# Kernel optimization log

Hardware: AMD Instinct MI355X
Metric: run time of the kernel (lower is better)

The kernel has to match this reference:

```python
import jax, jax.numpy as jnp
import numpy as np

B, T, C = 16, 4096, 128
CODEBOOK_SIZE = 1024


def setup_inputs() -> dict:
    key = jax.random.key(0)
    kx, ke = jax.random.split(key)
    x = jax.random.normal(kx, (B, T, C), dtype=jnp.float32)
    embed = jax.random.normal(ke, (CODEBOOK_SIZE, C), dtype=jnp.float32)
    return {"x": x, "embed": embed}


def reference(x, embed):
    # x: [B, T, C], embed: [K, C]
    b, t, c = x.shape
    flat = x.reshape(b * t, c)                      # [BT, C]
    # distance = -||x - e||^2, expanded so we never materialize [BT, K, C]
    x_sq = jnp.sum(flat * flat, axis=-1, keepdims=True)   # [BT, 1]
    e_sq = jnp.sum(embed * embed, axis=-1)                 # [K]
    dist = 2.0 * (flat @ embed.T) - x_sq - e_sq[None, :]   # [BT, K]
    embed_ind = jnp.argmax(dist, axis=-1).reshape(b, t)    # [B, T]
    quantized = embed[embed_ind]                           # [B, T, C] gather
    return quantized, embed_ind
```

## Files before the change

kernel.cpp:

```cpp
#include <hip/hip_runtime.h>
#include <float.h>


#define Cdim        128
#define KCODES      1024
#define CH          32
#define NCH         32
#define BROWS       128
#define THREADS     256
#define IMG_OFF     4096
#define CHUNK_BYTES 16384

typedef _Float16 f16;
typedef __attribute__((ext_vector_type(8))) _Float16 f16x8;
typedef __attribute__((ext_vector_type(4))) float    f32x4;

#define MFMA16(A, B, C) __builtin_amdgcn_mfma_f32_16x16x32_f16((A), (B), (C), 0, 0, 0)

__global__ __launch_bounds__(256) void esq_kernel(const float* __restrict__ embed,
                                                  float* __restrict__ esq, int K) {
    int gid  = blockIdx.x * blockDim.x + threadIdx.x;
    int code = gid >> 6;
    int lane = threadIdx.x & 63;
    if (code >= K) return;
    float2 v = ((const float2*)(embed + (size_t)code * Cdim))[lane];
    float  s = fmaf(v.x, v.x, v.y * v.y);
    #pragma unroll
    for (int m = 32; m >= 1; m >>= 1) s += __shfl_xor(s, m, 64);
    if (lane == 0) esq[code] = s;
}

__device__ __forceinline__ void cvt8s(float4 a, float4 b, float scale,
                                      f16x8& h, f16x8& lo) {
    float v[8] = {a.x, a.y, a.z, a.w, b.x, b.y, b.z, b.w};
    #pragma unroll
    for (int i = 0; i < 8; ++i) {
        float s = v[i] * scale;
        f16 hh = (f16)s;
        h[i]  = hh;
        lo[i] = (f16)(s - (float)hh);
    }
}

__global__ __launch_bounds__(256) void bconv_kernel(const float* __restrict__ embed,
                                                    char* __restrict__ ws) {
    int t    = blockIdx.x * 256 + threadIdx.x;
    int code = t >> 4;
    int seg  = t & 15;
    int ks   = seg >> 2;
    int kseg = seg & 3;
    int ch = code >> 5, ct = (code >> 4) & 1, lr = code & 15;
    const float4* p = (const float4*)(embed + (size_t)code * Cdim + ks * 32 + kseg * 8);
    f16x8 h, lo;
    cvt8s(p[0], p[1], 1.0f, h, lo);
    size_t base = (size_t)IMG_OFF + (size_t)ch * CHUNK_BYTES
                + (ct * 4 + ks) * 1024 + (kseg * 16 + lr) * 16;
    *(f16x8*)(ws + base)        = h;
    *(f16x8*)(ws + base + 8192) = lo;
}

__device__ __forceinline__ void gll16(const void* g, void* l) {
    __builtin_amdgcn_global_load_lds(
        (const __attribute__((address_space(1))) unsigned int*)g,
        (__attribute__((address_space(3))) unsigned int*)l, 16, 0, 0);
}

__global__ __launch_bounds__(THREADS, 2) void vq_kernel(
    const float* __restrict__ x, const float* __restrict__ embed,
    const char* __restrict__ ws, float* __restrict__ outq,
    float* __restrict__ outi) {

    __shared__ __align__(16) char Bb[3][CHUNK_BYTES];

    const int tid  = threadIdx.x;
    const int wid  = tid >> 6;
    const int l    = tid & 63;
    const int lr   = l & 15;
    const int lg   = l >> 4;
    const int row0 = blockIdx.x * BROWS;
    const int wrow = row0 + wid * 32;

    #pragma unroll
    for (int b = 0; b < 2; ++b) {
        const char* src = ws + IMG_OFF + b * CHUNK_BYTES + wid * 4096 + (size_t)l * 16;
        char*       dst = &Bb[b][wid * 4096];
        #pragma unroll
        for (int i = 0; i < 4; ++i) gll16(src + i * 1024, dst + i * 1024);
    }

    f16x8 bxh[2][4], bxl[2][4];
    #pragma unroll
    for (int rt = 0; rt < 2; ++rt) {
        const float* xr = x + (size_t)(wrow + rt * 16 + lr) * Cdim + lg * 8;
        #pragma unroll
        for (int ks = 0; ks < 4; ++ks) {
            float4 v0 = *(const float4*)(xr + ks * 32);
            float4 v1 = *(const float4*)(xr + ks * 32 + 4);
            cvt8s(v0, v1, 2.0f, bxh[rt][ks], bxl[rt][ks]);
        }
    }

    const float* esqp = (const float*)ws;

    float best[2] = {-FLT_MAX, -FLT_MAX};
    int   bidx[2] = {0, 0};
    int cur = 0, pf = 2;

    #pragma unroll 1
    for (int ch = 0; ch < NCH; ++ch) {
        if (ch == NCH - 1) asm volatile("s_waitcnt vmcnt(0)" ::: "memory");
        else               asm volatile("s_waitcnt vmcnt(4)" ::: "memory");
        __builtin_amdgcn_s_barrier();

        if (ch + 2 < NCH) {
            const char* src = ws + IMG_OFF + (size_t)(ch + 2) * CHUNK_BYTES
                            + wid * 4096 + (size_t)l * 16;
            char* dst = &Bb[0][0] + (size_t)pf * CHUNK_BYTES + wid * 4096;
            #pragma unroll
            for (int i = 0; i < 4; ++i) gll16(src + i * 1024, dst + i * 1024);
        }

        f32x4 acc[2][2];
        #pragma unroll
        for (int ct = 0; ct < 2; ++ct)
            #pragma unroll
            for (int rt = 0; rt < 2; ++rt)
                acc[ct][rt] = (f32x4){0.f, 0.f, 0.f, 0.f};

        const char* bb = &Bb[0][0] + (size_t)cur * CHUNK_BYTES + (size_t)l * 16;

        #pragma unroll
        for (int ks = 0; ks < 4; ++ks) {
            f16x8 eh0 = *(const f16x8*)(bb + ks * 1024);
            f16x8 el0 = *(const f16x8*)(bb + ks * 1024 + 8192);
            f16x8 eh1 = *(const f16x8*)(bb + (4 + ks) * 1024);
            f16x8 el1 = *(const f16x8*)(bb + (4 + ks) * 1024 + 8192);

            __builtin_amdgcn_s_setprio(1);
            acc[0][0] = MFMA16(eh0, bxh[0][ks], acc[0][0]);
            acc[0][1] = MFMA16(eh0, bxh[1][ks], acc[0][1]);
            acc[1][0] = MFMA16(eh1, bxh[0][ks], acc[1][0]);
            acc[1][1] = MFMA16(eh1, bxh[1][ks], acc[1][1]);
            acc[0][0] = MFMA16(eh0, bxl[0][ks], acc[0][0]);
            acc[0][1] = MFMA16(eh0, bxl[1][ks], acc[0][1]);
            acc[1][0] = MFMA16(eh1, bxl[0][ks], acc[1][0]);
            acc[1][1] = MFMA16(eh1, bxl[1][ks], acc[1][1]);
            acc[0][0] = MFMA16(el0, bxh[0][ks], acc[0][0]);
            acc[0][1] = MFMA16(el0, bxh[1][ks], acc[0][1]);
            acc[1][0] = MFMA16(el1, bxh[0][ks], acc[1][0]);
            acc[1][1] = MFMA16(el1, bxh[1][ks], acc[1][1]);
            __builtin_amdgcn_s_setprio(0);
        }

        #pragma unroll
        for (int ct = 0; ct < 2; ++ct) {
            const int cb = ch * CH + ct * 16 + lg * 4;
            float4 e4 = *(const float4*)(esqp + cb);
            #pragma unroll
            for (int rt = 0; rt < 2; ++rt)
                #pragma unroll
                for (int j = 0; j < 4; ++j) {
                    float s = acc[ct][rt][j] - ((const float*)&e4)[j];
                    if (s > best[rt]) { best[rt] = s; bidx[rt] = cb + j; }
                }
        }

        cur = (cur == 2) ? 0 : cur + 1;
        pf  = (pf  == 2) ? 0 : pf  + 1;
    }

    __syncthreads();
    int* winners = (int*)&Bb[0][0];
    #pragma unroll
    for (int rt = 0; rt < 2; ++rt) {
        float bs = best[rt]; int bi = bidx[rt];
        #pragma unroll
        for (int m = 16; m <= 32; m <<= 1) {
            float vs = __shfl_xor(bs, m, 64);
            int   vi = __shfl_xor(bi, m, 64);
            if (vs > bs || (vs == bs && vi < bi)) { bs = vs; bi = vi; }
        }
        if (lg == 0) {
            winners[wid * 32 + rt * 16 + lr] = bi;
            outi[wrow + rt * 16 + lr] = (float)bi;
        }
    }
    __syncthreads();

    #pragma unroll
    for (int i = 0; i < 16; ++i) {
        int pos = i * THREADS + tid;
        int r = pos >> 5, c4 = pos & 31;
        int idx = winners[r];
        float4 v = ((const float4*)(embed + (size_t)idx * Cdim))[c4];
        ((float4*)(outq + (size_t)(row0 + r) * Cdim))[c4] = v;
    }
}

extern "C" void kernel_launch(void* const* d_in, const int* in_sizes, int n_in,
                              void* d_out, int out_size, void* d_ws, size_t ws_size,
                              hipStream_t stream) {
    const float* x     = (const float*)d_in[0];
    const float* embed = (const float*)d_in[1];
    const int M = in_sizes[0] / Cdim;
    const int K = in_sizes[1] / Cdim;
    float* outq = (float*)d_out;
    float* outi = outq + (size_t)M * Cdim;

    esq_kernel <<<K / 4, 256, 0, stream>>>(embed, (float*)d_ws, K);
    bconv_kernel<<<64, 256, 0, stream>>>(embed, (char*)d_ws);
    vq_kernel  <<<M / BROWS, THREADS, 0, stream>>>(x, embed, (const char*)d_ws,
                                                   outq, outi);
}
```

Baseline: 62.43 us.

## Split codebook tiles across waves and software-pipeline MFMA with argmax scoring

Each wave now handles 64 rows and one 16-code half of every chunk, instead of 32 rows and both halves. This halves the per-wave LDS reads of codebook fragments per MFMA and doubles the register-held x fragments. The chunk loop is unrolled with two accumulator sets, so scoring of one chunk overlaps the MFMAs of the next. Squared norms are staged in LDS rather than read from global memory. A cross-wave merge through LDS picks the final argmin. Register pressure rises (16+16 f16x8 x fragments plus 8 accumulators), which may reduce occupancy.

```diff
diff --git a/kernel.cpp b/kernel.cpp
--- a/kernel.cpp
+++ b/kernel.cpp
@@ -49,12 +49,12 @@
     int seg  = t & 15;
     int ks   = seg >> 2;
     int kseg = seg & 3;
-    int ch = code >> 5, ct = (code >> 4) & 1, lr = code & 15;
+    int ch = code >> 5, nt = (code >> 4) & 1, lr = code & 15;
     const float4* p = (const float4*)(embed + (size_t)code * Cdim + ks * 32 + kseg * 8);
     f16x8 h, lo;
     cvt8s(p[0], p[1], 1.0f, h, lo);
     size_t base = (size_t)IMG_OFF + (size_t)ch * CHUNK_BYTES
-                + (ct * 4 + ks) * 1024 + (kseg * 16 + lr) * 16;
+                + nt * 4096 + ks * 1024 + (kseg * 16 + lr) * 16;
     *(f16x8*)(ws + base)        = h;
     *(f16x8*)(ws + base + 8192) = lo;
 }
@@ -70,16 +70,19 @@
     const char* __restrict__ ws, float* __restrict__ outq,
     float* __restrict__ outi) {
 
-    __shared__ __align__(16) char Bb[3][CHUNK_BYTES];
+    __shared__ __align__(16) char  Bb[3][CHUNK_BYTES];
+    __shared__ __align__(16) float esq_lds[KCODES];
 
     const int tid  = threadIdx.x;
     const int wid  = tid >> 6;
     const int l    = tid & 63;
     const int lr   = l & 15;
     const int lg   = l >> 4;
+    const int wr   = wid & 1;
+    const int nt   = wid >> 1;
     const int row0 = blockIdx.x * BROWS;
-    const int wrow = row0 + wid * 32;
-
+
+    gll16(ws + wid * 1024 + (size_t)l * 16, (char*)esq_lds + wid * 1024);
     #pragma unroll
     for (int b = 0; b < 2; ++b) {
         const char* src = ws + IMG_OFF + b * CHUNK_BYTES + wid * 4096 + (size_t)l * 16;
@@ -88,10 +91,10 @@
         for (int i = 0; i < 4; ++i) gll16(src + i * 1024, dst + i * 1024);
     }
 
-    f16x8 bxh[2][4], bxl[2][4];
-    #pragma unroll
-    for (int rt = 0; rt < 2; ++rt) {
-        const float* xr = x + (size_t)(wrow + rt * 16 + lr) * Cdim + lg * 8;
+    f16x8 bxh[4][4], bxl[4][4];
+    #pragma unroll
+    for (int rt = 0; rt < 4; ++rt) {
+        const float* xr = x + (size_t)(row0 + wr * 64 + rt * 16 + lr) * Cdim + lg * 8;
         #pragma unroll
         for (int ks = 0; ks < 4; ++ks) {
             float4 v0 = *(const float4*)(xr + ks * 32);
@@ -100,14 +103,14 @@
         }
     }
 
-    const float* esqp = (const float*)ws;
-
-    float best[2] = {-FLT_MAX, -FLT_MAX};
-    int   bidx[2] = {0, 0};
+    float best[4];
+    int   bidx[4];
+    #pragma unroll
+    for (int rt = 0; rt < 4; ++rt) { best[rt] = -FLT_MAX; bidx[rt] = 0; }
+
     int cur = 0, pf = 2;
 
-    #pragma unroll 1
-    for (int ch = 0; ch < NCH; ++ch) {
+    auto compute = [&](int ch, f32x4* acc) {
         if (ch == NCH - 1) asm volatile("s_waitcnt vmcnt(0)" ::: "memory");
         else               asm volatile("s_waitcnt vmcnt(4)" ::: "memory");
         __builtin_amdgcn_s_barrier();
@@ -120,59 +123,61 @@
             for (int i = 0; i < 4; ++i) gll16(src + i * 1024, dst + i * 1024);
         }
 
-        f32x4 acc[2][2];
-        #pragma unroll
-        for (int ct = 0; ct < 2; ++ct)
-            #pragma unroll
-            for (int rt = 0; rt < 2; ++rt)
-                acc[ct][rt] = (f32x4){0.f, 0.f, 0.f, 0.f};
-
-        const char* bb = &Bb[0][0] + (size_t)cur * CHUNK_BYTES + (size_t)l * 16;
-
+        #pragma unroll
+        for (int rt = 0; rt < 4; ++rt) acc[rt] = (f32x4){0.f, 0.f, 0.f, 0.f};
+
+        const char* bb = &Bb[0][0] + (size_t)cur * CHUNK_BYTES
+                       + nt * 4096 + (size_t)l * 16;
         #pragma unroll
         for (int ks = 0; ks < 4; ++ks) {
-            f16x8 eh0 = *(const f16x8*)(bb + ks * 1024);
-            f16x8 el0 = *(const f16x8*)(bb + ks * 1024 + 8192);
-            f16x8 eh1 = *(const f16x8*)(bb + (4 + ks) * 1024);
-            f16x8 el1 = *(const f16x8*)(bb + (4 + ks) * 1024 + 8192);
-
+            f16x8 eh = *(const f16x8*)(bb + ks * 1024);
+            f16x8 el = *(const f16x8*)(bb + ks * 1024 + 8192);
             __builtin_amdgcn_s_setprio(1);
-            acc[0][0] = MFMA16(eh0, bxh[0][ks], acc[0][0]);
-            acc[0][1] = MFMA16(eh0, bxh[1][ks], acc[0][1]);
-            acc[1][0] = MFMA16(eh1, bxh[0][ks], acc[1][0]);
-            acc[1][1] = MFMA16(eh1, bxh[1][ks], acc[1][1]);
-            acc[0][0] = MFMA16(eh0, bxl[0][ks], acc[0][0]);
-            acc[0][1] = MFMA16(eh0, bxl[1][ks], acc[0][1]);
-            acc[1][0] = MFMA16(eh1, bxl[0][ks], acc[1][0]);
-            acc[1][1] = MFMA16(eh1, bxl[1][ks], acc[1][1]);
-            acc[0][0] = MFMA16(el0, bxh[0][ks], acc[0][0]);
-            acc[0][1] = MFMA16(el0, bxh[1][ks], acc[0][1]);
-            acc[1][0] = MFMA16(el1, bxh[0][ks], acc[1][0]);
-            acc[1][1] = MFMA16(el1, bxh[1][ks], acc[1][1]);
+            #pragma unroll
+            for (int rt = 0; rt < 4; ++rt) acc[rt] = MFMA16(eh, bxh[rt][ks], acc[rt]);
+            #pragma unroll
+            for (int rt = 0; rt < 4; ++rt) acc[rt] = MFMA16(eh, bxl[rt][ks], acc[rt]);
+            #pragma unroll
+            for (int rt = 0; rt < 4; ++rt) acc[rt] = MFMA16(el, bxh[rt][ks], acc[rt]);
             __builtin_amdgcn_s_setprio(0);
-        }
-
-        #pragma unroll
-        for (int ct = 0; ct < 2; ++ct) {
-            const int cb = ch * CH + ct * 16 + lg * 4;
-            float4 e4 = *(const float4*)(esqp + cb);
-            #pragma unroll
-            for (int rt = 0; rt < 2; ++rt)
-                #pragma unroll
-                for (int j = 0; j < 4; ++j) {
-                    float s = acc[ct][rt][j] - ((const float*)&e4)[j];
-                    if (s > best[rt]) { best[rt] = s; bidx[rt] = cb + j; }
-                }
         }
 
         cur = (cur == 2) ? 0 : cur + 1;
         pf  = (pf  == 2) ? 0 : pf  + 1;
-    }
+    };
+
+    auto score = [&](int ch, const f32x4* acc) {
+        const int cb = ch * CH + nt * 16 + lg * 4;
+        float4 e4 = *(const float4*)&esq_lds[cb];
+        #pragma unroll
+        for (int rt = 0; rt < 4; ++rt)
+            #pragma unroll
+            for (int j = 0; j < 4; ++j) {
+                float s = acc[rt][j] - ((const float*)&e4)[j];
+                if (s > best[rt]) { best[rt] = s; bidx[rt] = cb + j; }
+            }
+    };
+
+    f32x4 accA[4], accB[4];
+    compute(0, accA);
+    #pragma unroll 1
+    for (int b = 0; b < 15; ++b) {
+        compute(2 * b + 1, accB);
+        score  (2 * b,     accA);
+        compute(2 * b + 2, accA);
+        score  (2 * b + 1, accB);
+    }
+    compute(31, accB);
+    score  (30, accA);
+    score  (31, accB);
 
     __syncthreads();
-    int* winners = (int*)&Bb[0][0];
-    #pragma unroll
-    for (int rt = 0; rt < 2; ++rt) {
+    float* mrgv    = (float*)&Bb[0][0];
+    int*   mrgi    = (int*)  &Bb[0][4096];
+    int*   winners = (int*)  &Bb[0][8192];
+
+    #pragma unroll
+    for (int rt = 0; rt < 4; ++rt) {
         float bs = best[rt]; int bi = bidx[rt];
         #pragma unroll
         for (int m = 16; m <= 32; m <<= 1) {
@@ -181,9 +186,17 @@
             if (vs > bs || (vs == bs && vi < bi)) { bs = vs; bi = vi; }
         }
         if (lg == 0) {
-            winners[wid * 32 + rt * 16 + lr] = bi;
-            outi[wrow + rt * 16 + lr] = (float)bi;
-        }
+            mrgv[nt * BROWS + wr * 64 + rt * 16 + lr] = bs;
+            mrgi[nt * BROWS + wr * 64 + rt * 16 + lr] = bi;
+        }
+    }
+    __syncthreads();
+    if (tid < BROWS) {
+        float v0 = mrgv[tid];         int i0 = mrgi[tid];
+        float v1 = mrgv[BROWS + tid]; int i1 = mrgi[BROWS + tid];
+        int bi = (v1 > v0 || (v1 == v0 && i1 < i0)) ? i1 : i0;
+        winners[tid] = bi;
+        outi[row0 + tid] = (float)bi;
     }
     __syncthreads();
 
```

New measurement: 64.84 us. 1.04x slower.
